# Kernel optimization log

Measured on AMD Instinct MI355X. Metric: run time of the kernel, lower is better.

## Reference

```python
import jax, jax.numpy as jnp
import numpy as np

NU, N1, N2 = 100000, 60000, 60000   # users, domain-1 items, domain-2 items
E = 2000000                          # click edges per domain
DIN, DH, DOUT = 128, 128, 64


def setup_inputs() -> dict:
    key = jax.random.key(0)
    ks = jax.random.split(key, 14)
    emb = lambda k, shape: jax.random.normal(k, shape, dtype=jnp.float32) * 0.01
    w = lambda k, shape: jax.random.normal(k, shape, dtype=jnp.float32) * (1.0 / np.sqrt(shape[-2]))
    return {
        "emb_user": emb(ks[0], (NU, DIN)),
        "emb_d1": emb(ks[1], (N1, DIN)),
        "emb_d2": emb(ks[2], (N2, DIN)),
        # relation order: [user->d1 click, d1->user rev, user->d2 click, d2->user rev]
        "W_in": w(ks[3], (4, DIN, DH)),
        "b_in": jnp.zeros((4, DH), jnp.float32),
        "W_hid": w(ks[4], (4, DH, DH)),
        "b_hid": jnp.zeros((4, DH), jnp.float32),
        "W_out": w(ks[5], (4, DH, DOUT)),
        "b_out": jnp.zeros((4, DOUT), jnp.float32),
        "Wp_d1": jax.random.normal(ks[6], (DOUT, DOUT), dtype=jnp.float32),
        "Wp_d2": jax.random.normal(ks[7], (DOUT, DOUT), dtype=jnp.float32),
        "src_d1": jax.random.randint(ks[8], (E,), 0, NU, dtype=jnp.int32),
        "dst_d1": jax.random.randint(ks[9], (E,), 0, N1, dtype=jnp.int32),
        "src_d2": jax.random.randint(ks[10], (E,), 0, NU, dtype=jnp.int32),
        "dst_d2": jax.random.randint(ks[11], (E,), 0, N2, dtype=jnp.int32),
    }


def _gconv(x_src, W, b, src, dst, nsrc, ndst, n_dst):
    # DGL GraphConv, norm='both': D_dst^{-1/2} A D_src^{-1/2} (X W) + b
    m = (x_src * nsrc[:, None]) @ W                      # [N_src, dout]
    agg = jax.ops.segment_sum(m[src], dst, num_segments=n_dst)  # SpMM via gather/scatter
    return agg * ndst[:, None] + b


def reference(emb_user, emb_d1, emb_d2, W_in, b_in, W_hid, b_hid, W_out, b_out,
              Wp_d1, Wp_d2, src_d1, dst_d1, src_d2, dst_d2):
    Nu, Na, Nb = emb_user.shape[0], emb_d1.shape[0], emb_d2.shape[0]
    ones1 = jnp.ones(src_d1.shape[0], jnp.float32)
    ones2 = jnp.ones(src_d2.shape[0], jnp.float32)
    du1 = jax.ops.segment_sum(ones1, src_d1, num_segments=Nu)
    di1 = jax.ops.segment_sum(ones1, dst_d1, num_segments=Na)
    du2 = jax.ops.segment_sum(ones2, src_d2, num_segments=Nu)
    di2 = jax.ops.segment_sum(ones2, dst_d2, num_segments=Nb)
    r = lambda d: jax.lax.rsqrt(jnp.maximum(d, 1.0))
    nu1, ni1, nu2, ni2 = r(du1), r(di1), r(du2), r(di2)

    u, i1, i2 = emb_user, emb_d1, emb_d2
    layers = ((W_in, b_in, False), (W_hid, b_hid, False), (W_out, b_out, True))
    for W, b, last in layers:
        # HeteroGraphConv with aggregate='sum': user receives from both reverse relations
        u_new = (_gconv(i1, W[1], b[1], dst_d1, src_d1, ni1, nu1, Nu)
                 + _gconv(i2, W[3], b[3], dst_d2, src_d2, ni2, nu2, Nu))
        i1_new = _gconv(u, W[0], b[0], src_d1, dst_d1, nu1, ni1, Na)
        i2_new = _gconv(u, W[2], b[2], src_d2, dst_d2, nu2, ni2, Nb)
        if last:
            u, i1, i2 = u_new, i1_new, i2_new
        else:  # relu + dropout (eval mode: dropout is identity)
            u, i1, i2 = jax.nn.relu(u_new), jax.nn.relu(i1_new), jax.nn.relu(i2_new)

    # per-domain projection of user embeddings, then u_dot_v edge scoring
    u1 = u @ Wp_d1
    u2 = u @ Wp_d2
    s1 = jnp.sum(u1[src_d1] * i1[dst_d1], axis=-1)  # [E]
    s2 = jnp.sum(u2[src_d2] * i2[dst_d2], axis=-1)  # [E]
    return jnp.concatenate([s1, s2])
```

## Files before the change

kernel.cpp:

```cpp
#include <hip/hip_runtime.h>
#include <hip/hip_bf16.h>

typedef unsigned short ushort_t;
typedef __attribute__((ext_vector_type(8))) short bf16x8;
typedef __attribute__((ext_vector_type(4))) float f32x4;

constexpr int NU = 100000, N1 = 60000, N2 = 60000;
constexpr int E = 2000000;
constexpr int TOTN = 2 * NU + N1 + N2;
constexpr int NPART = 8;
constexpr int CH = 2048;
constexpr int NCHUNKS = (E + CH - 1) / CH;
constexpr int PSLICE = TOTN / NPART;
constexpr int NSUB = 8;
constexpr int SUBS = PSLICE / NSUB;

__device__ __forceinline__ ushort_t f2bf(float f) {
  unsigned u = __float_as_uint(f);
  u = u + 0x7fffu + ((u >> 16) & 1u);
  return (ushort_t)(u >> 16);
}

__global__ __launch_bounds__(256) void k_count(const int* __restrict__ s1,
                                               const int* __restrict__ d1,
                                               const int* __restrict__ s2,
                                               const int* __restrict__ d2,
                                               int* __restrict__ deg) {
  __shared__ int ls1[CH], ld1[CH], ls2[CH], ld2[CH];
  int part = blockIdx.x % NPART;
  int base = (blockIdx.x / NPART) * CH;
  int n = E - base; if (n > CH) n = CH;
  for (int i = threadIdx.x; i < n; i += 256) {
    ls1[i] = s1[base + i];
    ld1[i] = d1[base + i];
    ls2[i] = s2[base + i];
    ld2[i] = d2[base + i];
  }
  __syncthreads();
  int plo = part * PSLICE;
  for (int sub = 0; sub < NSUB; ++sub) {
    int lo = plo + sub * SUBS, hi = lo + SUBS;
    for (int i = threadIdx.x; i < n; i += 256) {
      int i0 = ls1[i];
      int i1 = NU + ld1[i];
      int i2 = NU + N1 + ls2[i];
      int i3 = 2 * NU + N1 + ld2[i];
      if (i0 >= lo && i0 < hi) atomicAdd(&deg[i0], 1);
      if (i1 >= lo && i1 < hi) atomicAdd(&deg[i1], 1);
      if (i2 >= lo && i2 < hi) atomicAdd(&deg[i2], 1);
      if (i3 >= lo && i3 < hi) atomicAdd(&deg[i3], 1);
    }
    __syncthreads();
  }
}

__global__ __launch_bounds__(256) void k_norm(const int* __restrict__ deg,
                                              float* __restrict__ nrm) {
  int i = blockIdx.x * 256 + threadIdx.x;
  if (i >= TOTN) return;
  int d = deg[i];
  nrm[i] = rsqrtf((float)(d > 1 ? d : 1));
}

__global__ __launch_bounds__(256) void k_scan(const int* __restrict__ deg,
                                              int* __restrict__ off,
                                              int* __restrict__ cur) {
  __shared__ int wsum[4];
  int seg = blockIdx.x;
  int baseIn, n, baseOut;
  if (seg == 0)      { baseIn = 0;            n = NU; baseOut = 0; }
  else if (seg == 1) { baseIn = NU;           n = N1; baseOut = NU + 1; }
  else if (seg == 2) { baseIn = NU + N1;      n = NU; baseOut = NU + N1 + 2; }
  else               { baseIn = 2 * NU + N1;  n = N2; baseOut = 2 * NU + N1 + 3; }
  const int* in = deg + baseIn;
  int* out = off + baseOut;
  int* curp = cur + baseIn;

  constexpr int ITEMS = 16;
  int t = threadIdx.x, lane = t & 63, wid = t >> 6;
  int carry = 0;
  for (int base = 0; base < n; base += 256 * ITEMS) {
    int vals[ITEMS];
    int lsum = 0;
    int i0 = base + t * ITEMS;
#pragma unroll
    for (int j = 0; j < ITEMS; ++j) {
      int i = i0 + j;
      int v = (i < n) ? in[i] : 0;
      vals[j] = v;
      lsum += v;
    }
    int incl = lsum;
#pragma unroll
    for (int d = 1; d < 64; d <<= 1) {
      int x = __shfl_up(incl, d, 64);
      if (lane >= d) incl += x;
    }
    if (lane == 63) wsum[wid] = incl;
    __syncthreads();
    int woff = 0;
    for (int w = 0; w < wid; ++w) woff += wsum[w];
    int chunkTotal = wsum[0] + wsum[1] + wsum[2] + wsum[3];
    int excl = carry + woff + (incl - lsum);
#pragma unroll
    for (int j = 0; j < ITEMS; ++j) {
      int i = i0 + j;
      if (i < n) { out[i] = excl; curp[i] = excl; }
      excl += vals[j];
    }
    carry += chunkTotal;
    __syncthreads();
  }
  if (t == 0) out[n] = carry;
}

__global__ __launch_bounds__(256) void k_fill(const int* __restrict__ s1,
                                              const int* __restrict__ d1,
                                              const int* __restrict__ s2,
                                              const int* __restrict__ d2,
                                              int* __restrict__ cur,
                                              int* __restrict__ a_s1,
                                              int* __restrict__ a_d1,
                                              int* __restrict__ a_s2,
                                              int* __restrict__ a_d2) {
  __shared__ int ls1[CH], ld1[CH], ls2[CH], ld2[CH];
  int part = blockIdx.x % NPART;
  int base = (blockIdx.x / NPART) * CH;
  int n = E - base; if (n > CH) n = CH;
  for (int i = threadIdx.x; i < n; i += 256) {
    ls1[i] = s1[base + i];
    ld1[i] = d1[base + i];
    ls2[i] = s2[base + i];
    ld2[i] = d2[base + i];
  }
  __syncthreads();
  int plo = part * PSLICE;
  for (int sub = 0; sub < NSUB; ++sub) {
    int lo = plo + sub * SUBS, hi = lo + SUBS;
    for (int i = threadIdx.x; i < n; i += 256) {
      int a = ls1[i], b = ld1[i];
      int i0 = a, i1 = NU + b;
      if (i0 >= lo && i0 < hi) a_s1[atomicAdd(&cur[i0], 1)] = b;
      if (i1 >= lo && i1 < hi) a_d1[atomicAdd(&cur[i1], 1)] = a;
      int c = ls2[i], d = ld2[i];
      int i2 = NU + N1 + c, i3 = 2 * NU + N1 + d;
      if (i2 >= lo && i2 < hi) a_s2[atomicAdd(&cur[i2], 1)] = d;
      if (i3 >= lo && i3 < hi) a_d2[atomicAdd(&cur[i3], 1)] = c;
    }
    __syncthreads();
  }
}

template <int K, int N, bool BF16OUT>
__global__ __launch_bounds__(256) void k_gemm(const float* __restrict__ A,
                                              const float* __restrict__ W,
                                              void* __restrict__ Cv, int M,
                                              const float* __restrict__ rowscale) {
  constexpr int KF = K / 32, NF = N / 16;
  __shared__ __align__(16) ushort_t sW[N * K];
  for (int i = threadIdx.x * 4; i < K * N; i += 1024) {
    float4 w4 = *(const float4*)&W[i];
    int k = i / N, n0 = i % N;
    float wv[4] = {w4.x, w4.y, w4.z, w4.w};
#pragma unroll
    for (int j = 0; j < 4; ++j) {
      int n = n0 + j;
      sW[(n * K + k) ^ ((n & 7) << 3)] = f2bf(wv[j]);
    }
  }
  __syncthreads();

  int w = threadIdx.x >> 6, lane = threadIdx.x & 63;
  int col = lane & 15, kg = lane >> 4;
  int r = blockIdx.x * 64 + w * 16 + col;
  int rA = r < M ? r : M - 1;

  bf16x8 af[KF];
#pragma unroll
  for (int kf = 0; kf < KF; ++kf) {
    const float* ap = &A[(size_t)rA * K + kf * 32 + kg * 8];
    float4 lo = *(const float4*)ap;
    float4 hi = *(const float4*)(ap + 4);
    bf16x8 v;
    v[0] = (short)f2bf(lo.x); v[1] = (short)f2bf(lo.y);
    v[2] = (short)f2bf(lo.z); v[3] = (short)f2bf(lo.w);
    v[4] = (short)f2bf(hi.x); v[5] = (short)f2bf(hi.y);
    v[6] = (short)f2bf(hi.z); v[7] = (short)f2bf(hi.w);
    af[kf] = v;
  }

  f32x4 acc[NF] = {};
#pragma unroll
  for (int nf = 0; nf < NF; ++nf) {
    int n = nf * 16 + col;
#pragma unroll
    for (int kf = 0; kf < KF; ++kf) {
      int idx = (n * K + kf * 32 + kg * 8) ^ ((n & 7) << 3);
      bf16x8 bfrag = *(const bf16x8*)&sW[idx];
      acc[nf] = __builtin_amdgcn_mfma_f32_16x16x32_bf16(af[kf], bfrag, acc[nf], 0, 0, 0);
    }
  }

  int orow = blockIdx.x * 64 + w * 16 + kg * 4;
#pragma unroll
  for (int reg = 0; reg < 4; ++reg) {
    int R = orow + reg;
    if (R >= M) break;
    float sc = rowscale ? rowscale[R] : 1.f;
#pragma unroll
    for (int nf = 0; nf < NF; ++nf) {
      float v = sc * acc[nf][reg];
      size_t o = (size_t)R * N + nf * 16 + col;
      if constexpr (BF16OUT) ((ushort_t*)Cv)[o] = f2bf(v);
      else                   ((float*)Cv)[o] = v;
    }
  }
}

template <int D, bool ACCUM, bool RELU>
__global__ __launch_bounds__(256) void k_gather(const ushort_t* __restrict__ z,
                                                const int* __restrict__ off,
                                                const int* __restrict__ adj,
                                                const float* __restrict__ ndst,
                                                const float* __restrict__ bias,
                                                const float* __restrict__ bias2,
                                                float* __restrict__ out, int nv) {
  constexpr int LPN = D / 4;
  constexpr int NPB = 256 / LPN;
  int t = threadIdx.x;
  int slot = t / LPN, l = t % LPN;
  int v = blockIdx.x * NPB + slot;
  if (v >= nv) return;
  int e0 = off[v], e1 = off[v + 1];
  float a0 = 0.f, a1 = 0.f, a2 = 0.f, a3 = 0.f;
  auto addp = [&](uint2 p) {
    a0 += __uint_as_float(p.x << 16);
    a1 += __uint_as_float(p.x & 0xffff0000u);
    a2 += __uint_as_float(p.y << 16);
    a3 += __uint_as_float(p.y & 0xffff0000u);
  };
  int e = e0;
  for (; e + 4 <= e1; e += 4) {
    int sA = adj[e], sB = adj[e + 1], sC = adj[e + 2], sD = adj[e + 3];
    uint2 pA = *(const uint2*)&z[(size_t)sA * D + 4 * l];
    uint2 pB = *(const uint2*)&z[(size_t)sB * D + 4 * l];
    uint2 pC = *(const uint2*)&z[(size_t)sC * D + 4 * l];
    uint2 pD = *(const uint2*)&z[(size_t)sD * D + 4 * l];
    addp(pA); addp(pB); addp(pC); addp(pD);
  }
  for (; e < e1; ++e) {
    int s = adj[e];
    addp(*(const uint2*)&z[(size_t)s * D + 4 * l]);
  }
  float nd = ndst[v];
  size_t o = (size_t)v * D + 4 * l;
  float r0, r1, r2, r3;
  if constexpr (ACCUM) {
    float4 old = *(const float4*)&out[o];
    r0 = old.x + nd * a0; r1 = old.y + nd * a1;
    r2 = old.z + nd * a2; r3 = old.w + nd * a3;
  } else {
    float b0 = bias[4 * l], b1 = bias[4 * l + 1], b2 = bias[4 * l + 2], b3 = bias[4 * l + 3];
    if (bias2) {
      b0 += bias2[4 * l]; b1 += bias2[4 * l + 1];
      b2 += bias2[4 * l + 2]; b3 += bias2[4 * l + 3];
    }
    r0 = nd * a0 + b0; r1 = nd * a1 + b1; r2 = nd * a2 + b2; r3 = nd * a3 + b3;
  }
  if constexpr (RELU) {
    r0 = fmaxf(r0, 0.f); r1 = fmaxf(r1, 0.f);
    r2 = fmaxf(r2, 0.f); r3 = fmaxf(r3, 0.f);
  }
  float4 res; res.x = r0; res.y = r1; res.z = r2; res.w = r3;
  *(float4*)&out[o] = res;
}

__global__ __launch_bounds__(256) void k_score(const float* __restrict__ u,
                                               const float* __restrict__ it,
                                               const int* __restrict__ src,
                                               const int* __restrict__ dst,
                                               float* __restrict__ out, int ne) {
  int e = blockIdx.x * 256 + threadIdx.x;
  if (e >= ne) return;
  const float4* a = (const float4*)(u + (size_t)src[e] * 64);
  const float4* b = (const float4*)(it + (size_t)dst[e] * 64);
  float s = 0.f;
#pragma unroll
  for (int j = 0; j < 16; ++j) {
    float4 x = a[j], y = b[j];
    s += x.x * y.x + x.y * y.y + x.z * y.z + x.w * y.w;
  }
  out[e] = s;
}

extern "C" void kernel_launch(void* const* d_in, const int* in_sizes, int n_in,
                              void* d_out, int out_size, void* d_ws, size_t ws_size,
                              hipStream_t stream) {
  const float* emb_user = (const float*)d_in[0];
  const float* emb_d1   = (const float*)d_in[1];
  const float* emb_d2   = (const float*)d_in[2];
  const float* W_in     = (const float*)d_in[3];
  const float* b_in     = (const float*)d_in[4];
  const float* W_hid    = (const float*)d_in[5];
  const float* b_hid    = (const float*)d_in[6];
  const float* W_out    = (const float*)d_in[7];
  const float* b_out    = (const float*)d_in[8];
  const float* Wp_d1    = (const float*)d_in[9];
  const float* Wp_d2    = (const float*)d_in[10];
  const int* src_d1     = (const int*)d_in[11];
  const int* dst_d1     = (const int*)d_in[12];
  const int* src_d2     = (const int*)d_in[13];
  const int* dst_d2     = (const int*)d_in[14];
  float* out = (float*)d_out;

  char* p = (char*)d_ws;
  auto alloc = [&](size_t bytes) {
    void* r = (void*)p;
    p += (bytes + 15) & ~(size_t)15;
    return r;
  };
  float* bufU[2] = {(float*)alloc((size_t)NU * 128 * 4), (float*)alloc((size_t)NU * 128 * 4)};
  float* bufI1 = (float*)alloc((size_t)N1 * 128 * 4);
  float* bufI2 = (float*)alloc((size_t)N2 * 128 * 4);
  ushort_t* m = (ushort_t*)alloc((size_t)NU * 128 * 2);
  float* nrm = (float*)alloc((size_t)TOTN * 4);
  int* deg = (int*)alloc((size_t)TOTN * 4);
  int* off = (int*)alloc((size_t)(TOTN + 4) * 4);
  int* cur = (int*)alloc((size_t)TOTN * 4);
  int* adj_s1 = (int*)alloc((size_t)E * 4);
  int* adj_d1 = (int*)alloc((size_t)E * 4);
  int* adj_s2 = (int*)alloc((size_t)E * 4);
  int* adj_d2 = (int*)alloc((size_t)E * 4);

  if ((size_t)(p - (char*)d_ws) > ws_size) return;

  const float* nu1 = nrm;
  const float* ni1 = nrm + NU;
  const float* nu2 = nrm + NU + N1;
  const float* ni2 = nrm + 2 * NU + N1;
  const int* off_u1 = off;
  const int* off_i1 = off + NU + 1;
  const int* off_u2 = off + NU + N1 + 2;
  const int* off_i2 = off + 2 * NU + N1 + 3;

  int gE = (E + 255) / 256;

  hipMemsetAsync(deg, 0, (size_t)TOTN * 4, stream);
  k_count<<<NCHUNKS * NPART, 256, 0, stream>>>(src_d1, dst_d1, src_d2, dst_d2, deg);
  k_norm<<<(TOTN + 255) / 256, 256, 0, stream>>>(deg, nrm);
  k_scan<<<4, 256, 0, stream>>>(deg, off, cur);
  k_fill<<<NCHUNKS * NPART, 256, 0, stream>>>(src_d1, dst_d1, src_d2, dst_d2, cur,
                                              adj_s1, adj_d1, adj_s2, adj_d2);

  const float* U = emb_user;
  const float* I1 = emb_d1;
  const float* I2 = emb_d2;
  for (int L = 0; L < 3; ++L) {
    const float* W = L == 0 ? W_in : L == 1 ? W_hid : W_out;
    const float* B = L == 0 ? b_in : L == 1 ? b_hid : b_out;
    float* uNew = bufU[L % 2];
    if (L < 2) {
      constexpr int Nc = 128;
      k_gemm<128, Nc, true><<<(N1 + 63) / 64, 256, 0, stream>>>(I1, W + 1 * 128 * Nc, m, N1, ni1);
      k_gather<Nc, false, false><<<(NU + 7) / 8, 256, 0, stream>>>(
          m, off_u1, adj_s1, nu1, B + 1 * Nc, B + 3 * Nc, uNew, NU);
      k_gemm<128, Nc, true><<<(N2 + 63) / 64, 256, 0, stream>>>(I2, W + 3 * 128 * Nc, m, N2, ni2);
      k_gather<Nc, true, true><<<(NU + 7) / 8, 256, 0, stream>>>(
          m, off_u2, adj_s2, nu2, nullptr, nullptr, uNew, NU);
      k_gemm<128, Nc, true><<<(NU + 63) / 64, 256, 0, stream>>>(U, W + 0 * 128 * Nc, m, NU, nu1);
      k_gather<Nc, false, true><<<(N1 + 7) / 8, 256, 0, stream>>>(
          m, off_i1, adj_d1, ni1, B + 0 * Nc, nullptr, bufI1, N1);
      k_gemm<128, Nc, true><<<(NU + 63) / 64, 256, 0, stream>>>(U, W + 2 * 128 * Nc, m, NU, nu2);
      k_gather<Nc, false, true><<<(N2 + 7) / 8, 256, 0, stream>>>(
          m, off_i2, adj_d2, ni2, B + 2 * Nc, nullptr, bufI2, N2);
    } else {
      constexpr int Nc = 64;
      k_gemm<128, Nc, true><<<(N1 + 63) / 64, 256, 0, stream>>>(I1, W + 1 * 128 * Nc, m, N1, ni1);
      k_gather<Nc, false, false><<<(NU + 15) / 16, 256, 0, stream>>>(
          m, off_u1, adj_s1, nu1, B + 1 * Nc, B + 3 * Nc, uNew, NU);
      k_gemm<128, Nc, true><<<(N2 + 63) / 64, 256, 0, stream>>>(I2, W + 3 * 128 * Nc, m, N2, ni2);
      k_gather<Nc, true, false><<<(NU + 15) / 16, 256, 0, stream>>>(
          m, off_u2, adj_s2, nu2, nullptr, nullptr, uNew, NU);
      k_gemm<128, Nc, true><<<(NU + 63) / 64, 256, 0, stream>>>(U, W + 0 * 128 * Nc, m, NU, nu1);
      k_gather<Nc, false, false><<<(N1 + 15) / 16, 256, 0, stream>>>(
          m, off_i1, adj_d1, ni1, B + 0 * Nc, nullptr, bufI1, N1);
      k_gemm<128, Nc, true><<<(NU + 63) / 64, 256, 0, stream>>>(U, W + 2 * 128 * Nc, m, NU, nu2);
      k_gather<Nc, false, false><<<(N2 + 15) / 16, 256, 0, stream>>>(
          m, off_i2, adj_d2, ni2, B + 2 * Nc, nullptr, bufI2, N2);
    }
    U = uNew;
    I1 = bufI1;
    I2 = bufI2;
  }

  float* u1 = bufU[1];
  float* u2 = bufU[1] + (size_t)NU * 64;
  k_gemm<64, 64, false><<<(NU + 63) / 64, 256, 0, stream>>>(U, Wp_d1, u1, NU, nullptr);
  k_gemm<64, 64, false><<<(NU + 63) / 64, 256, 0, stream>>>(U, Wp_d2, u2, NU, nullptr);
  k_score<<<gE, 256, 0, stream>>>(u1, I1, src_d1, dst_d1, out, E);
  k_score<<<gE, 256, 0, stream>>>(u2, I2, src_d2, dst_d2, out + E, E);
}
```

Baseline: 2.892 ms.

## Fuse dual-relation user gather, store activations in bf16, score edges per user via CSR

Merges the two reverse-relation user aggregations into one gather kernel, so the user output is written once instead of accumulated through a read-modify-write pass. Hidden activations are kept in bf16, which halves intermediate traffic and lets the GEMMs load A directly without converting. Edge scoring is regrouped by source user: the fill step also records original edge ids, and a wave-per-user kernel reuses the user row and scatters scores back by edge id. In exchange it adds two edge-id arrays and their writes during the fill, does scattered 4-byte output writes, and loses precision on the intermediate activations.

```diff
diff --git a/kernel.cpp b/kernel.cpp
--- a/kernel.cpp
+++ b/kernel.cpp
@@ -122,7 +122,9 @@
                                               int* __restrict__ a_s1,
                                               int* __restrict__ a_d1,
                                               int* __restrict__ a_s2,
-                                              int* __restrict__ a_d2) {
+                                              int* __restrict__ a_d2,
+                                              int* __restrict__ e_s1,
+                                              int* __restrict__ e_s2) {
   __shared__ int ls1[CH], ld1[CH], ls2[CH], ld2[CH];
   int part = blockIdx.x % NPART;
   int base = (blockIdx.x / NPART) * CH;
@@ -140,19 +142,41 @@
     for (int i = threadIdx.x; i < n; i += 256) {
       int a = ls1[i], b = ld1[i];
       int i0 = a, i1 = NU + b;
-      if (i0 >= lo && i0 < hi) a_s1[atomicAdd(&cur[i0], 1)] = b;
+      if (i0 >= lo && i0 < hi) {
+        int pos = atomicAdd(&cur[i0], 1);
+        a_s1[pos] = b;
+        e_s1[pos] = base + i;
+      }
       if (i1 >= lo && i1 < hi) a_d1[atomicAdd(&cur[i1], 1)] = a;
       int c = ls2[i], d = ld2[i];
       int i2 = NU + N1 + c, i3 = 2 * NU + N1 + d;
-      if (i2 >= lo && i2 < hi) a_s2[atomicAdd(&cur[i2], 1)] = d;
+      if (i2 >= lo && i2 < hi) {
+        int pos = atomicAdd(&cur[i2], 1);
+        a_s2[pos] = d;
+        e_s2[pos] = base + i;
+      }
       if (i3 >= lo && i3 < hi) a_d2[atomicAdd(&cur[i3], 1)] = c;
     }
     __syncthreads();
   }
 }
 
-template <int K, int N, bool BF16OUT>
-__global__ __launch_bounds__(256) void k_gemm(const float* __restrict__ A,
+__device__ __forceinline__ bf16x8 loadA8(const float* p) {
+  float4 lo = *(const float4*)p;
+  float4 hi = *(const float4*)(p + 4);
+  bf16x8 v;
+  v[0] = (short)f2bf(lo.x); v[1] = (short)f2bf(lo.y);
+  v[2] = (short)f2bf(lo.z); v[3] = (short)f2bf(lo.w);
+  v[4] = (short)f2bf(hi.x); v[5] = (short)f2bf(hi.y);
+  v[6] = (short)f2bf(hi.z); v[7] = (short)f2bf(hi.w);
+  return v;
+}
+__device__ __forceinline__ bf16x8 loadA8(const ushort_t* p) {
+  return *(const bf16x8*)p;
+}
+
+template <typename AT, int K, int N, bool BF16OUT>
+__global__ __launch_bounds__(256) void k_gemm(const AT* __restrict__ A,
                                               const float* __restrict__ W,
                                               void* __restrict__ Cv, int M,
                                               const float* __restrict__ rowscale) {
@@ -177,17 +201,8 @@
 
   bf16x8 af[KF];
 #pragma unroll
-  for (int kf = 0; kf < KF; ++kf) {
-    const float* ap = &A[(size_t)rA * K + kf * 32 + kg * 8];
-    float4 lo = *(const float4*)ap;
-    float4 hi = *(const float4*)(ap + 4);
-    bf16x8 v;
-    v[0] = (short)f2bf(lo.x); v[1] = (short)f2bf(lo.y);
-    v[2] = (short)f2bf(lo.z); v[3] = (short)f2bf(lo.w);
-    v[4] = (short)f2bf(hi.x); v[5] = (short)f2bf(hi.y);
-    v[6] = (short)f2bf(hi.z); v[7] = (short)f2bf(hi.w);
-    af[kf] = v;
-  }
+  for (int kf = 0; kf < KF; ++kf)
+    af[kf] = loadA8(&A[(size_t)rA * K + kf * 32 + kg * 8]);
 
   f32x4 acc[NF] = {};
 #pragma unroll
@@ -217,27 +232,15 @@
   }
 }
 
-template <int D, bool ACCUM, bool RELU>
-__global__ __launch_bounds__(256) void k_gather(const ushort_t* __restrict__ z,
-                                                const int* __restrict__ off,
-                                                const int* __restrict__ adj,
-                                                const float* __restrict__ ndst,
-                                                const float* __restrict__ bias,
-                                                const float* __restrict__ bias2,
-                                                float* __restrict__ out, int nv) {
-  constexpr int LPN = D / 4;
-  constexpr int NPB = 256 / LPN;
-  int t = threadIdx.x;
-  int slot = t / LPN, l = t % LPN;
-  int v = blockIdx.x * NPB + slot;
-  if (v >= nv) return;
-  int e0 = off[v], e1 = off[v + 1];
-  float a0 = 0.f, a1 = 0.f, a2 = 0.f, a3 = 0.f;
+template <int D>
+__device__ __forceinline__ void accum_list(const ushort_t* __restrict__ z,
+                                           const int* __restrict__ adj,
+                                           int e0, int e1, int l, float4& A) {
   auto addp = [&](uint2 p) {
-    a0 += __uint_as_float(p.x << 16);
-    a1 += __uint_as_float(p.x & 0xffff0000u);
-    a2 += __uint_as_float(p.y << 16);
-    a3 += __uint_as_float(p.y & 0xffff0000u);
+    A.x += __uint_as_float(p.x << 16);
+    A.y += __uint_as_float(p.x & 0xffff0000u);
+    A.z += __uint_as_float(p.y << 16);
+    A.w += __uint_as_float(p.y & 0xffff0000u);
   };
   int e = e0;
   for (; e + 4 <= e1; e += 4) {
@@ -248,49 +251,114 @@
     uint2 pD = *(const uint2*)&z[(size_t)sD * D + 4 * l];
     addp(pA); addp(pB); addp(pC); addp(pD);
   }
-  for (; e < e1; ++e) {
-    int s = adj[e];
-    addp(*(const uint2*)&z[(size_t)s * D + 4 * l]);
-  }
+  for (; e < e1; ++e)
+    addp(*(const uint2*)&z[(size_t)adj[e] * D + 4 * l]);
+}
+
+template <int D, bool RELU, bool BF16OUT>
+__global__ __launch_bounds__(256) void k_gather(const ushort_t* __restrict__ z,
+                                                const int* __restrict__ off,
+                                                const int* __restrict__ adj,
+                                                const float* __restrict__ ndst,
+                                                const float* __restrict__ bias,
+                                                void* __restrict__ outv, int nv) {
+  constexpr int LPN = D / 4;
+  constexpr int NPB = 256 / LPN;
+  int t = threadIdx.x;
+  int slot = t / LPN, l = t % LPN;
+  int v = blockIdx.x * NPB + slot;
+  if (v >= nv) return;
+  float4 A = {0.f, 0.f, 0.f, 0.f};
+  accum_list<D>(z, adj, off[v], off[v + 1], l, A);
   float nd = ndst[v];
-  size_t o = (size_t)v * D + 4 * l;
-  float r0, r1, r2, r3;
-  if constexpr (ACCUM) {
-    float4 old = *(const float4*)&out[o];
-    r0 = old.x + nd * a0; r1 = old.y + nd * a1;
-    r2 = old.z + nd * a2; r3 = old.w + nd * a3;
-  } else {
-    float b0 = bias[4 * l], b1 = bias[4 * l + 1], b2 = bias[4 * l + 2], b3 = bias[4 * l + 3];
-    if (bias2) {
-      b0 += bias2[4 * l]; b1 += bias2[4 * l + 1];
-      b2 += bias2[4 * l + 2]; b3 += bias2[4 * l + 3];
-    }
-    r0 = nd * a0 + b0; r1 = nd * a1 + b1; r2 = nd * a2 + b2; r3 = nd * a3 + b3;
-  }
+  float r0 = nd * A.x + bias[4 * l];
+  float r1 = nd * A.y + bias[4 * l + 1];
+  float r2 = nd * A.z + bias[4 * l + 2];
+  float r3 = nd * A.w + bias[4 * l + 3];
   if constexpr (RELU) {
     r0 = fmaxf(r0, 0.f); r1 = fmaxf(r1, 0.f);
     r2 = fmaxf(r2, 0.f); r3 = fmaxf(r3, 0.f);
   }
-  float4 res; res.x = r0; res.y = r1; res.z = r2; res.w = r3;
-  *(float4*)&out[o] = res;
-}
-
-__global__ __launch_bounds__(256) void k_score(const float* __restrict__ u,
-                                               const float* __restrict__ it,
-                                               const int* __restrict__ src,
-                                               const int* __restrict__ dst,
-                                               float* __restrict__ out, int ne) {
-  int e = blockIdx.x * 256 + threadIdx.x;
-  if (e >= ne) return;
-  const float4* a = (const float4*)(u + (size_t)src[e] * 64);
-  const float4* b = (const float4*)(it + (size_t)dst[e] * 64);
-  float s = 0.f;
-#pragma unroll
-  for (int j = 0; j < 16; ++j) {
-    float4 x = a[j], y = b[j];
-    s += x.x * y.x + x.y * y.y + x.z * y.z + x.w * y.w;
-  }
-  out[e] = s;
+  size_t o = (size_t)v * D + 4 * l;
+  if constexpr (BF16OUT) {
+    uint2 pk;
+    pk.x = (unsigned)f2bf(r0) | ((unsigned)f2bf(r1) << 16);
+    pk.y = (unsigned)f2bf(r2) | ((unsigned)f2bf(r3) << 16);
+    *(uint2*)&((ushort_t*)outv)[o] = pk;
+  } else {
+    float4 res; res.x = r0; res.y = r1; res.z = r2; res.w = r3;
+    *(float4*)&((float*)outv)[o] = res;
+  }
+}
+
+template <int D, bool RELU>
+__global__ __launch_bounds__(256) void k_gather2(const ushort_t* __restrict__ z1,
+                                                 const ushort_t* __restrict__ z2,
+                                                 const int* __restrict__ off1,
+                                                 const int* __restrict__ adj1,
+                                                 const int* __restrict__ off2,
+                                                 const int* __restrict__ adj2,
+                                                 const float* __restrict__ nd1,
+                                                 const float* __restrict__ nd2,
+                                                 const float* __restrict__ b1,
+                                                 const float* __restrict__ b2,
+                                                 ushort_t* __restrict__ out, int nv) {
+  constexpr int LPN = D / 4;
+  constexpr int NPB = 256 / LPN;
+  int t = threadIdx.x;
+  int slot = t / LPN, l = t % LPN;
+  int v = blockIdx.x * NPB + slot;
+  if (v >= nv) return;
+  float4 A = {0.f, 0.f, 0.f, 0.f};
+  float4 B = {0.f, 0.f, 0.f, 0.f};
+  accum_list<D>(z1, adj1, off1[v], off1[v + 1], l, A);
+  accum_list<D>(z2, adj2, off2[v], off2[v + 1], l, B);
+  float n1 = nd1[v], n2 = nd2[v];
+  float r0 = n1 * A.x + n2 * B.x + b1[4 * l]     + b2[4 * l];
+  float r1 = n1 * A.y + n2 * B.y + b1[4 * l + 1] + b2[4 * l + 1];
+  float r2 = n1 * A.z + n2 * B.z + b1[4 * l + 2] + b2[4 * l + 2];
+  float r3 = n1 * A.w + n2 * B.w + b1[4 * l + 3] + b2[4 * l + 3];
+  if constexpr (RELU) {
+    r0 = fmaxf(r0, 0.f); r1 = fmaxf(r1, 0.f);
+    r2 = fmaxf(r2, 0.f); r3 = fmaxf(r3, 0.f);
+  }
+  uint2 pk;
+  pk.x = (unsigned)f2bf(r0) | ((unsigned)f2bf(r1) << 16);
+  pk.y = (unsigned)f2bf(r2) | ((unsigned)f2bf(r3) << 16);
+  *(uint2*)&out[(size_t)v * D + 4 * l] = pk;
+}
+
+__global__ __launch_bounds__(256) void k_score2(const float* __restrict__ up,
+                                                const float* __restrict__ ip,
+                                                const int* __restrict__ off,
+                                                const int* __restrict__ adj,
+                                                const int* __restrict__ eid,
+                                                float* __restrict__ out, int nu) {
+  int w = threadIdx.x >> 6, lane = threadIdx.x & 63;
+  int u = blockIdx.x * 4 + w;
+  if (u >= nu) return;
+  float uc = up[(size_t)u * 64 + lane];
+  int e0 = off[u], e1 = off[u + 1];
+  int e = e0;
+  for (; e + 2 <= e1; e += 2) {
+    int sA = adj[e], sB = adj[e + 1];
+    int idA = eid[e], idB = eid[e + 1];
+    float pA = uc * ip[(size_t)sA * 64 + lane];
+    float pB = uc * ip[(size_t)sB * 64 + lane];
+#pragma unroll
+    for (int d = 32; d >= 1; d >>= 1) {
+      pA += __shfl_xor(pA, d, 64);
+      pB += __shfl_xor(pB, d, 64);
+    }
+    if (lane == 0) { out[idA] = pA; out[idB] = pB; }
+  }
+  if (e < e1) {
+    int s = adj[e], id = eid[e];
+    float p = uc * ip[(size_t)s * 64 + lane];
+#pragma unroll
+    for (int d = 32; d >= 1; d >>= 1) p += __shfl_xor(p, d, 64);
+    if (lane == 0) out[id] = p;
+  }
 }
 
 extern "C" void kernel_launch(void* const* d_in, const int* in_sizes, int n_in,
@@ -319,10 +387,11 @@
     p += (bytes + 15) & ~(size_t)15;
     return r;
   };
-  float* bufU[2] = {(float*)alloc((size_t)NU * 128 * 4), (float*)alloc((size_t)NU * 128 * 4)};
-  float* bufI1 = (float*)alloc((size_t)N1 * 128 * 4);
-  float* bufI2 = (float*)alloc((size_t)N2 * 128 * 4);
-  ushort_t* m = (ushort_t*)alloc((size_t)NU * 128 * 2);
+  ushort_t* bufU[2] = {(ushort_t*)alloc((size_t)NU * 128 * 2),
+                       (ushort_t*)alloc((size_t)NU * 128 * 2)};
+  void* bufI1 = alloc((size_t)N1 * 128 * 2);
+  void* bufI2 = alloc((size_t)N2 * 128 * 2);
+  ushort_t* m = (ushort_t*)alloc((size_t)(N1 + N2) * 128 * 2);
   float* nrm = (float*)alloc((size_t)TOTN * 4);
   int* deg = (int*)alloc((size_t)TOTN * 4);
   int* off = (int*)alloc((size_t)(TOTN + 4) * 4);
@@ -331,6 +400,8 @@
   int* adj_d1 = (int*)alloc((size_t)E * 4);
   int* adj_s2 = (int*)alloc((size_t)E * 4);
   int* adj_d2 = (int*)alloc((size_t)E * 4);
+  int* eid_s1 = (int*)alloc((size_t)E * 4);
+  int* eid_s2 = (int*)alloc((size_t)E * 4);
 
   if ((size_t)(p - (char*)d_ws) > ws_size) return;
 
@@ -343,60 +414,60 @@
   const int* off_u2 = off + NU + N1 + 2;
   const int* off_i2 = off + 2 * NU + N1 + 3;
 
-  int gE = (E + 255) / 256;
-
   hipMemsetAsync(deg, 0, (size_t)TOTN * 4, stream);
   k_count<<<NCHUNKS * NPART, 256, 0, stream>>>(src_d1, dst_d1, src_d2, dst_d2, deg);
   k_norm<<<(TOTN + 255) / 256, 256, 0, stream>>>(deg, nrm);
   k_scan<<<4, 256, 0, stream>>>(deg, off, cur);
   k_fill<<<NCHUNKS * NPART, 256, 0, stream>>>(src_d1, dst_d1, src_d2, dst_d2, cur,
-                                              adj_s1, adj_d1, adj_s2, adj_d2);
-
-  const float* U = emb_user;
-  const float* I1 = emb_d1;
-  const float* I2 = emb_d2;
-  for (int L = 0; L < 3; ++L) {
-    const float* W = L == 0 ? W_in : L == 1 ? W_hid : W_out;
-    const float* B = L == 0 ? b_in : L == 1 ? b_hid : b_out;
-    float* uNew = bufU[L % 2];
-    if (L < 2) {
-      constexpr int Nc = 128;
-      k_gemm<128, Nc, true><<<(N1 + 63) / 64, 256, 0, stream>>>(I1, W + 1 * 128 * Nc, m, N1, ni1);
-      k_gather<Nc, false, false><<<(NU + 7) / 8, 256, 0, stream>>>(
-          m, off_u1, adj_s1, nu1, B + 1 * Nc, B + 3 * Nc, uNew, NU);
-      k_gemm<128, Nc, true><<<(N2 + 63) / 64, 256, 0, stream>>>(I2, W + 3 * 128 * Nc, m, N2, ni2);
-      k_gather<Nc, true, true><<<(NU + 7) / 8, 256, 0, stream>>>(
-          m, off_u2, adj_s2, nu2, nullptr, nullptr, uNew, NU);
-      k_gemm<128, Nc, true><<<(NU + 63) / 64, 256, 0, stream>>>(U, W + 0 * 128 * Nc, m, NU, nu1);
-      k_gather<Nc, false, true><<<(N1 + 7) / 8, 256, 0, stream>>>(
-          m, off_i1, adj_d1, ni1, B + 0 * Nc, nullptr, bufI1, N1);
-      k_gemm<128, Nc, true><<<(NU + 63) / 64, 256, 0, stream>>>(U, W + 2 * 128 * Nc, m, NU, nu2);
-      k_gather<Nc, false, true><<<(N2 + 7) / 8, 256, 0, stream>>>(
-          m, off_i2, adj_d2, ni2, B + 2 * Nc, nullptr, bufI2, N2);
-    } else {
-      constexpr int Nc = 64;
-      k_gemm<128, Nc, true><<<(N1 + 63) / 64, 256, 0, stream>>>(I1, W + 1 * 128 * Nc, m, N1, ni1);
-      k_gather<Nc, false, false><<<(NU + 15) / 16, 256, 0, stream>>>(
-          m, off_u1, adj_s1, nu1, B + 1 * Nc, B + 3 * Nc, uNew, NU);
-      k_gemm<128, Nc, true><<<(N2 + 63) / 64, 256, 0, stream>>>(I2, W + 3 * 128 * Nc, m, N2, ni2);
-      k_gather<Nc, true, false><<<(NU + 15) / 16, 256, 0, stream>>>(
-          m, off_u2, adj_s2, nu2, nullptr, nullptr, uNew, NU);
-      k_gemm<128, Nc, true><<<(NU + 63) / 64, 256, 0, stream>>>(U, W + 0 * 128 * Nc, m, NU, nu1);
-      k_gather<Nc, false, false><<<(N1 + 15) / 16, 256, 0, stream>>>(
-          m, off_i1, adj_d1, ni1, B + 0 * Nc, nullptr, bufI1, N1);
-      k_gemm<128, Nc, true><<<(NU + 63) / 64, 256, 0, stream>>>(U, W + 2 * 128 * Nc, m, NU, nu2);
-      k_gather<Nc, false, false><<<(N2 + 15) / 16, 256, 0, stream>>>(
-          m, off_i2, adj_d2, ni2, B + 2 * Nc, nullptr, bufI2, N2);
-    }
-    U = uNew;
-    I1 = bufI1;
-    I2 = bufI2;
-  }
-
-  float* u1 = bufU[1];
-  float* u2 = bufU[1] + (size_t)NU * 64;
-  k_gemm<64, 64, false><<<(NU + 63) / 64, 256, 0, stream>>>(U, Wp_d1, u1, NU, nullptr);
-  k_gemm<64, 64, false><<<(NU + 63) / 64, 256, 0, stream>>>(U, Wp_d2, u2, NU, nullptr);
-  k_score<<<gE, 256, 0, stream>>>(u1, I1, src_d1, dst_d1, out, E);
-  k_score<<<gE, 256, 0, stream>>>(u2, I2, src_d2, dst_d2, out + E, E);
-}
+                                              adj_s1, adj_d1, adj_s2, adj_d2,
+                                              eid_s1, eid_s2);
+
+  ushort_t* mI1 = m;
+  ushort_t* mI2 = m + (size_t)N1 * 128;
+  ushort_t* mI1h = m;
+  ushort_t* mI2h = m + (size_t)N1 * 64;
+  ushort_t* mU = m;
+
+  k_gemm<float, 128, 128, true><<<(N1 + 63) / 64, 256, 0, stream>>>(emb_d1, W_in + 1 * 128 * 128, mI1, N1, ni1);
+  k_gemm<float, 128, 128, true><<<(N2 + 63) / 64, 256, 0, stream>>>(emb_d2, W_in + 3 * 128 * 128, mI2, N2, ni2);
+  k_gather2<128, true><<<(NU + 7) / 8, 256, 0, stream>>>(
+      mI1, mI2, off_u1, adj_s1, off_u2, adj_s2, nu1, nu2,
+      b_in + 1 * 128, b_in + 3 * 128, bufU[0], NU);
+  k_gemm<float, 128, 128, true><<<(NU + 63) / 64, 256, 0, stream>>>(emb_user, W_in + 0 * 128 * 128, mU, NU, nu1);
+  k_gather<128, true, true><<<(N1 + 7) / 8, 256, 0, stream>>>(
+      mU, off_i1, adj_d1, ni1, b_in + 0 * 128, bufI1, N1);
+  k_gemm<float, 128, 128, true><<<(NU + 63) / 64, 256, 0, stream>>>(emb_user, W_in + 2 * 128 * 128, mU, NU, nu2);
+  k_gather<128, true, true><<<(N2 + 7) / 8, 256, 0, stream>>>(
+      mU, off_i2, adj_d2, ni2, b_in + 2 * 128, bufI2, N2);
+
+  k_gemm<ushort_t, 128, 128, true><<<(N1 + 63) / 64, 256, 0, stream>>>((ushort_t*)bufI1, W_hid + 1 * 128 * 128, mI1, N1, ni1);
+  k_gemm<ushort_t, 128, 128, true><<<(N2 + 63) / 64, 256, 0, stream>>>((ushort_t*)bufI2, W_hid + 3 * 128 * 128, mI2, N2, ni2);
+  k_gather2<128, true><<<(NU + 7) / 8, 256, 0, stream>>>(
+      mI1, mI2, off_u1, adj_s1, off_u2, adj_s2, nu1, nu2,
+      b_hid + 1 * 128, b_hid + 3 * 128, bufU[1], NU);
+  k_gemm<ushort_t, 128, 128, true><<<(NU + 63) / 64, 256, 0, stream>>>(bufU[0], W_hid + 0 * 128 * 128, mU, NU, nu1);
+  k_gather<128, true, true><<<(N1 + 7) / 8, 256, 0, stream>>>(
+      mU, off_i1, adj_d1, ni1, b_hid + 0 * 128, bufI1, N1);
+  k_gemm<ushort_t, 128, 128, true><<<(NU + 63) / 64, 256, 0, stream>>>(bufU[0], W_hid + 2 * 128 * 128, mU, NU, nu2);
+  k_gather<128, true, true><<<(N2 + 7) / 8, 256, 0, stream>>>(
+      mU, off_i2, adj_d2, ni2, b_hid + 2 * 128, bufI2, N2);
+
+  k_gemm<ushort_t, 128, 64, true><<<(N1 + 63) / 64, 256, 0, stream>>>((ushort_t*)bufI1, W_out + 1 * 128 * 64, mI1h, N1, ni1);
+  k_gemm<ushort_t, 128, 64, true><<<(N2 + 63) / 64, 256, 0, stream>>>((ushort_t*)bufI2, W_out + 3 * 128 * 64, mI2h, N2, ni2);
+  k_gather2<64, false><<<(NU + 15) / 16, 256, 0, stream>>>(
+      mI1h, mI2h, off_u1, adj_s1, off_u2, adj_s2, nu1, nu2,
+      b_out + 1 * 64, b_out + 3 * 64, bufU[0], NU);
+  k_gemm<ushort_t, 128, 64, true><<<(NU + 63) / 64, 256, 0, stream>>>(bufU[1], W_out + 0 * 128 * 64, mU, NU, nu1);
+  k_gather<64, false, false><<<(N1 + 15) / 16, 256, 0, stream>>>(
+      mU, off_i1, adj_d1, ni1, b_out + 0 * 64, bufI1, N1);
+  k_gemm<ushort_t, 128, 64, true><<<(NU + 63) / 64, 256, 0, stream>>>(bufU[1], W_out + 2 * 128 * 64, mU, NU, nu2);
+  k_gather<64, false, false><<<(N2 + 15) / 16, 256, 0, stream>>>(
+      mU, off_i2, adj_d2, ni2, b_out + 2 * 64, bufI2, N2);
+
+  float* u1 = (float*)m;
+  float* u2 = (float*)bufU[1];
+  k_gemm<ushort_t, 64, 64, false><<<(NU + 63) / 64, 256, 0, stream>>>(bufU[0], Wp_d1, u1, NU, nullptr);
+  k_gemm<ushort_t, 64, 64, false><<<(NU + 63) / 64, 256, 0, stream>>>(bufU[0], Wp_d2, u2, NU, nullptr);
+  k_score2<<<(NU + 3) / 4, 256, 0, stream>>>(u1, (const float*)bufI1, off_u1, adj_s1, eid_s1, out, NU);
+  k_score2<<<(NU + 3) / 4, 256, 0, stream>>>(u2, (const float*)bufI2, off_u2, adj_s2, eid_s2, out + E, NU);
+}
```

Result: faster. 2.386 ms (-17.5%).
